# Kernel tuning notes

Hardware: AMD Instinct MI355X
Metric: run time of the kernel (lower is better)

## Reference

```python
import jax, jax.numpy as jnp
from jax import lax
import numpy as np

ALPHA = 1.5
N_ITER = 50  # default n_iter of entmax_bisect
NUM_HEADS = 16


def _entmax_bisect_p(X):
    """entmax-bisect over last axis (Peters et al. 2019 bisection algorithm)."""
    a = ALPHA
    inv = 1.0 / (a - 1.0)  # = 2.0 for alpha=1.5
    Xa = X * (a - 1.0)
    d = X.shape[-1]
    max_val = jnp.max(Xa, axis=-1, keepdims=True)
    tau_lo = max_val - 1.0
    tau_hi = max_val - (1.0 / d) ** (a - 1.0)
    f_lo = jnp.sum(jnp.clip(Xa - tau_lo, 0.0) ** inv, axis=-1, keepdims=True) - 1.0
    dm0 = tau_hi - tau_lo

    def body(carry, _):
        tau_lo, dm, _ = carry
        dm = dm * 0.5
        tau_m = tau_lo + dm
        p_m = jnp.clip(Xa - tau_m, 0.0) ** inv
        f_m = jnp.sum(p_m, axis=-1, keepdims=True) - 1.0
        tau_lo = jnp.where(f_m * f_lo >= 0, tau_m, tau_lo)
        return (tau_lo, dm, tau_m), None

    (tau_lo, dm, tau_m), _ = lax.scan(body, (tau_lo, dm0, tau_lo), None, length=N_ITER)
    p = jnp.clip(Xa - tau_m, 0.0) ** inv
    return p / jnp.sum(p, axis=-1, keepdims=True)  # ensure_sum_one


@jax.custom_vjp
def entmax_bisect(X):
    return _entmax_bisect_p(X)


def _entmax_fwd(X):
    p = _entmax_bisect_p(X)
    return p, p


def _entmax_bwd(p, dY):
    # exact entmax Jacobian-vector product (matches entmax package backward)
    gppr = jnp.where(p > 0, p ** (2.0 - ALPHA), 0.0)
    dX = dY * gppr
    q = jnp.sum(dX, axis=-1, keepdims=True) / jnp.sum(gppr, axis=-1, keepdims=True)
    return (dX - q * gppr,)


entmax_bisect.defvjp(_entmax_fwd, _entmax_bwd)


def setup_inputs() -> dict:
    key = jax.random.key(0)
    ks = jax.random.split(key, 9)
    B, N, C = 4, 1024, 1024
    s = 0.02
    return {
        "x": jax.random.normal(ks[0], (B, N, C), dtype=jnp.float32),
        "Wq": jax.random.normal(ks[1], (C, C), dtype=jnp.float32) * s,
        "bq": jnp.zeros((C,), dtype=jnp.float32),
        "Wk": jax.random.normal(ks[2], (C, C), dtype=jnp.float32) * s,
        "bk": jnp.zeros((C,), dtype=jnp.float32),
        "Wv": jax.random.normal(ks[3], (C, C), dtype=jnp.float32) * s,
        "bv": jnp.zeros((C,), dtype=jnp.float32),
        "Wo": jax.random.normal(ks[4], (C, C), dtype=jnp.float32) * s,
        "bo": jnp.zeros((C,), dtype=jnp.float32),
    }


def reference(x, Wq, bq, Wk, bk, Wv, bv, Wo, bo):
    B, N, C = x.shape
    H = NUM_HEADS
    Dh = C // H

    def split_heads(t):  # [B,N,C] -> [B,H,N,Dh]
        return t.reshape(B, N, H, Dh).transpose(0, 2, 1, 3)

    q = split_heads(x @ Wq + bq)
    k = split_heads(x @ Wk + bk)
    v = split_heads(x @ Wv + bv)

    scores = jnp.einsum("bhnd,bhmd->bhnm", q, k) / (float(Dh) ** 0.5)
    attn = entmax_bisect(scores)  # [B,H,N,N], sparse simplex weights
    out = jnp.einsum("bhnm,bhmd->bhnd", attn, v)
    out = out.transpose(0, 2, 1, 3).reshape(B, N, C)
    return out @ Wo + bo, attn
```

## Files before the change

### kernel.cpp

```cpp
#include <hip/hip_runtime.h>
#include <hip/hip_bf16.h>
#include <stdint.h>

#define NBAT 4
#define SEQ 1024
#define CH 1024
#define NH 16
#define DH 64
#define MTOT (NBAT*SEQ)

typedef __attribute__((ext_vector_type(8))) short bf16x8;
typedef __attribute__((ext_vector_type(4))) float f32x4;
typedef unsigned short u16;

#define FENCE() asm volatile("" ::: "memory")
#define BAR() do { FENCE(); __builtin_amdgcn_s_barrier(); FENCE(); } while (0)
#define WAIT_VM0() asm volatile("s_waitcnt vmcnt(0)" ::: "memory")
#define WAIT_VM2() asm volatile("s_waitcnt vmcnt(2)" ::: "memory")
#define WAIT_VM6() asm volatile("s_waitcnt vmcnt(6)" ::: "memory")
#define WAIT_LGKM0() asm volatile("s_waitcnt lgkmcnt(0)" ::: "memory")

__device__ __forceinline__ void g2l16(void* lds, const void* g) {
  __builtin_amdgcn_global_load_lds(
      (const __attribute__((address_space(1))) uint32_t*)g,
      (__attribute__((address_space(3))) uint32_t*)lds, 16, 0, 0);
}

__device__ __forceinline__ u16 f2bf(float f) {
  union { float f; uint32_t u; } v; v.f = f;
  uint32_t lsb = (v.u >> 16) & 1u;
  v.u += 0x7fffu + lsb;
  return (u16)(v.u >> 16);
}

__device__ __forceinline__ bf16x8 ldfrag(const u16* base, int row, int koff) {
  return *(const bf16x8*)((const char*)base + row * 128 + (koff ^ ((row & 7) << 4)));
}

__global__ __launch_bounds__(256) void cvt_x(const float* __restrict__ x,
                                             u16* __restrict__ xb) {
  int i = blockIdx.x * 256 + threadIdx.x;
  float4 v = ((const float4*)x)[i];
  ushort4 o;
  o.x = f2bf(v.x); o.y = f2bf(v.y); o.z = f2bf(v.z); o.w = f2bf(v.w);
  ((ushort4*)xb)[i] = o;
}

__global__ __launch_bounds__(256) void wt_bf16(const float* __restrict__ W,
                                               u16* __restrict__ Wt) {
  __shared__ u16 tile[64][65];
  const int bi = blockIdx.x;
  const int bj = blockIdx.y;
  const int t = threadIdx.x;
  const int c4 = (t & 15) * 4, rr = t >> 4;
#pragma unroll
  for (int p = 0; p < 4; p++) {
    int r = p * 16 + rr;
    float4 v = *(const float4*)(W + (size_t)(bj * 64 + r) * CH + bi * 64 + c4);
    tile[r][c4 + 0] = f2bf(v.x); tile[r][c4 + 1] = f2bf(v.y);
    tile[r][c4 + 2] = f2bf(v.z); tile[r][c4 + 3] = f2bf(v.w);
  }
  __syncthreads();
  const int n = t >> 2, ks = (t & 3) * 16;
  u16 tmp[16];
#pragma unroll
  for (int i = 0; i < 16; i++) tmp[i] = tile[ks + i][n];
#pragma unroll
  for (int s = 0; s < 4; s++) {
    ushort4 o; o.x = tmp[4*s]; o.y = tmp[4*s+1]; o.z = tmp[4*s+2]; o.w = tmp[4*s+3];
    *(ushort4*)(Wt + (size_t)(bi * 64 + n) * CH + bj * 64 + ks + 4 * s) = o;
  }
}

template<int MODE>
__global__ __launch_bounds__(256) void gemm128(
    const u16* __restrict__ A, const u16* __restrict__ Bt,
    const float* __restrict__ bias, void* __restrict__ outp)
{
  __shared__ u16 As[128 * 32];
  __shared__ u16 Bs[128 * 32];
  const int t = threadIdx.x;
  const int bn0 = blockIdx.x * 128;
  const int bm0 = blockIdx.y * 128;
  const int wid = t >> 6, lane = t & 63;
  const int wr = wid >> 1, wc = wid & 1;
  const int cl = lane & 15, g = lane >> 4;

  f32x4 acc[4][4] = {};
  const u16* ga = A  + (size_t)(bm0 + (t >> 2)) * CH + (t & 3) * 8;
  const u16* gb = Bt + (size_t)(bn0 + (t >> 2)) * CH + (t & 3) * 8;

  for (int k0 = 0; k0 < CH; k0 += 32) {
    g2l16(As + t * 8,        ga + k0);
    g2l16(As + 2048 + t * 8, ga + (size_t)64 * CH + k0);
    g2l16(Bs + t * 8,        gb + k0);
    g2l16(Bs + 2048 + t * 8, gb + (size_t)64 * CH + k0);
    __syncthreads();
    bf16x8 af[4], bfr[4];
#pragma unroll
    for (int f = 0; f < 4; f++) {
      af[f]  = *(const bf16x8*)(As + (wr * 64 + f * 16 + cl) * 32 + g * 8);
      bfr[f] = *(const bf16x8*)(Bs + (wc * 64 + f * 16 + cl) * 32 + g * 8);
    }
#pragma unroll
    for (int i = 0; i < 4; i++)
#pragma unroll
      for (int j = 0; j < 4; j++)
        acc[i][j] = __builtin_amdgcn_mfma_f32_16x16x32_bf16(af[i], bfr[j], acc[i][j], 0, 0, 0);
    __syncthreads();
  }

#pragma unroll
  for (int i = 0; i < 4; i++)
#pragma unroll
    for (int j = 0; j < 4; j++) {
      const int row0 = bm0 + wr * 64 + i * 16 + g * 4;
      const int col  = bn0 + wc * 64 + j * 16 + cl;
      const float bb = bias[col];
      f32x4 v = acc[i][j];
      if (MODE == 0) {
        u16* o = (u16*)outp;
#pragma unroll
        for (int q = 0; q < 4; q++) o[(size_t)(row0 + q) * CH + col] = f2bf(v[q] + bb);
      } else if (MODE == 1) {
        u16* o = (u16*)outp;
        ushort4 pk;
        pk.x = f2bf(v[0] + bb); pk.y = f2bf(v[1] + bb);
        pk.z = f2bf(v[2] + bb); pk.w = f2bf(v[3] + bb);
        *(ushort4*)(o + (size_t)col * MTOT + row0) = pk;
      } else {
        float* o = (float*)outp;
#pragma unroll
        for (int q = 0; q < 4; q++) o[(size_t)(row0 + q) * CH + col] = v[q] + bb;
      }
    }
}

__global__ __launch_bounds__(256, 3) void fused_attn(
    const u16* __restrict__ q, const u16* __restrict__ k,
    const u16* __restrict__ vt, float* __restrict__ attn,
    u16* __restrict__ o)
{
  __shared__ u16 buf[3][64 * 64];
  __shared__ u16 pcb[4 * 256];

  const int t = threadIdx.x;
  const int w = t >> 6, lane = t & 63;
  const int cl = lane & 15, g = lane >> 4;

  const int lin = blockIdx.x;
  const int u = lin >> 3;
  const int n0 = (u & 63) * 16;
  const int bh = (lin & 7) | ((u >> 6) << 3);
  const int b = bh >> 4, h = bh & 15;
  const int r0 = w * 4;

  const u16* qb = q  + ((size_t)(b * SEQ + n0) * CH + h * DH);
  const u16* kb = k  + ((size_t)(b * SEQ) * CH + h * DH);
  const u16* vb = vt + ((size_t)(h * DH) * MTOT + b * SEQ);

  const bf16x8 aq0 = *(const bf16x8*)(qb + (size_t)(r0 + (cl & 3)) * CH + g * 8);
  const bf16x8 aq1 = *(const bf16x8*)(qb + (size_t)(r0 + (cl & 3)) * CH + 32 + g * 8);

  const int srow = t >> 3;
  const int sbyte = ((t & 7) * 16) ^ ((srow & 7) << 4);
  const int scol = sbyte >> 1;

  g2l16(buf[0] + t * 8,        kb + (size_t)srow * CH + scol);
  g2l16(buf[0] + 2048 + t * 8, kb + (size_t)(srow + 32) * CH + scol);
  g2l16(buf[1] + t * 8,        kb + (size_t)(64 + srow) * CH + scol);
  g2l16(buf[1] + 2048 + t * 8, kb + (size_t)(64 + srow + 32) * CH + scol);

  float xa[4][16];

#pragma unroll
  for (int c = 0; c < 16; ++c) {
    WAIT_LGKM0();
    if (c < 15) { WAIT_VM2(); } else { WAIT_VM0(); }
    BAR();
    if (c + 2 < 16) {
      const u16* kc = kb + (size_t)(64 * (c + 2)) * CH;
      u16* d = buf[(c + 2) % 3];
      g2l16(d + t * 8,        kc + (size_t)srow * CH + scol);
      g2l16(d + 2048 + t * 8, kc + (size_t)(srow + 32) * CH + scol);
    }
    const u16* kc = buf[c % 3];
    f32x4 sc0 = {}, sc1 = {}, sc2 = {}, sc3 = {};
    sc0 = __builtin_amdgcn_mfma_f32_16x16x32_bf16(aq0, ldfrag(kc, cl,      g * 16), sc0, 0, 0, 0);
    sc0 = __builtin_amdgcn_mfma_f32_16x16x32_bf16(aq1, ldfrag(kc, cl,      64 + g * 16), sc0, 0, 0, 0);
    sc1 = __builtin_amdgcn_mfma_f32_16x16x32_bf16(aq0, ldfrag(kc, 16 + cl, g * 16), sc1, 0, 0, 0);
    sc1 = __builtin_amdgcn_mfma_f32_16x16x32_bf16(aq1, ldfrag(kc, 16 + cl, 64 + g * 16), sc1, 0, 0, 0);
    sc2 = __builtin_amdgcn_mfma_f32_16x16x32_bf16(aq0, ldfrag(kc, 32 + cl, g * 16), sc2, 0, 0, 0);
    sc2 = __builtin_amdgcn_mfma_f32_16x16x32_bf16(aq1, ldfrag(kc, 32 + cl, 64 + g * 16), sc2, 0, 0, 0);
    sc3 = __builtin_amdgcn_mfma_f32_16x16x32_bf16(aq0, ldfrag(kc, 48 + cl, g * 16), sc3, 0, 0, 0);
    sc3 = __builtin_amdgcn_mfma_f32_16x16x32_bf16(aq1, ldfrag(kc, 48 + cl, 64 + g * 16), sc3, 0, 0, 0);
#pragma unroll
    for (int qq = 0; qq < 4; ++qq) {
      float v = sc0[qq];
      v = (g == 1) ? sc1[qq] : v;
      v = (g == 2) ? sc2[qq] : v;
      v = (g == 3) ? sc3[qq] : v;
      xa[qq][c] = v * 0.0625f;
    }
  }

  g2l16(buf[1] + t * 8,        vb + (size_t)srow * MTOT + scol);
  g2l16(buf[1] + 2048 + t * 8, vb + (size_t)(srow + 32) * MTOT + scol);
  g2l16(buf[2] + t * 8,        vb + (size_t)srow * MTOT + 64 + scol);
  g2l16(buf[2] + 2048 + t * 8, vb + (size_t)(srow + 32) * MTOT + 64 + scol);

  float tau[4];
#pragma unroll
  for (int r = 0; r < 4; ++r) {
    float m = xa[r][0];
#pragma unroll
    for (int j = 1; j < 16; ++j) m = fmaxf(m, xa[r][j]);
#pragma unroll
    for (int off = 1; off < 64; off <<= 1) m = fmaxf(m, __shfl_xor(m, off));
    tau[r] = m - 1.0f;
  }
  for (int it = 0; it < 8; ++it) {
    float ss[4], sd[4];
#pragma unroll
    for (int r = 0; r < 4; ++r) {
      float s2 = 0.f, s1 = 0.f;
#pragma unroll
      for (int j = 0; j < 16; ++j) {
        float d = fmaxf(xa[r][j] - tau[r], 0.f);
        s2 = fmaf(d, d, s2); s1 += d;
      }
      ss[r] = s2; sd[r] = s1;
    }
#pragma unroll
    for (int off = 1; off < 64; off <<= 1) {
#pragma unroll
      for (int r = 0; r < 4; ++r) {
        ss[r] += __shfl_xor(ss[r], off);
        sd[r] += __shfl_xor(sd[r], off);
      }
    }
#pragma unroll
    for (int r = 0; r < 4; ++r)
      tau[r] += (ss[r] - 1.0f) / (sd[r] + sd[r]);
  }
  float inv[4];
#pragma unroll
  for (int r = 0; r < 4; ++r) {
    float s2 = 0.f;
#pragma unroll
    for (int j = 0; j < 16; ++j) { float d = fmaxf(xa[r][j] - tau[r], 0.f); s2 = fmaf(d, d, s2); }
#pragma unroll
    for (int off = 1; off < 64; off <<= 1) s2 += __shfl_xor(s2, off);
    inv[r] = 1.0f / s2;
  }

  char* pw = (char*)pcb + w * 512;
  f32x4 pva0 = {}, pva1 = {}, pva2 = {}, pva3 = {};
  float* ab = attn + (size_t)bh * SEQ * SEQ + (size_t)(n0 + r0) * SEQ;
#pragma unroll
  for (int vc = 0; vc < 16; ++vc) {
    float pval[4];
#pragma unroll
    for (int r = 0; r < 4; ++r) {
      float d = fmaxf(xa[r][vc] - tau[r], 0.f);
      pval[r] = d * d * inv[r];
      *(u16*)(pw + r * 128 + ((lane * 2) ^ (r << 4))) = f2bf(pval[r]);
    }
    WAIT_LGKM0();
    if (vc == 0) { WAIT_VM2(); } else { WAIT_VM6(); }
    BAR();
    if (vc + 2 < 16) {
      const u16* vc2 = vb + (size_t)64 * (vc + 2);
      u16* d = buf[(16 + vc + 2) % 3];
      g2l16(d + t * 8,        vc2 + (size_t)srow * MTOT + scol);
      g2l16(d + 2048 + t * 8, vc2 + (size_t)(srow + 32) * MTOT + scol);
    }
    const u16* vbu = buf[(16 + vc) % 3];
    const bf16x8 ap0 = *(const bf16x8*)(pw + (cl & 3) * 128 + ((g * 16) ^ ((cl & 3) << 4)));
    const bf16x8 ap1 = *(const bf16x8*)(pw + (cl & 3) * 128 + ((64 + g * 16) ^ ((cl & 3) << 4)));
    pva0 = __builtin_amdgcn_mfma_f32_16x16x32_bf16(ap0, ldfrag(vbu, cl,      g * 16), pva0, 0, 0, 0);
    pva0 = __builtin_amdgcn_mfma_f32_16x16x32_bf16(ap1, ldfrag(vbu, cl,      64 + g * 16), pva0, 0, 0, 0);
    pva1 = __builtin_amdgcn_mfma_f32_16x16x32_bf16(ap0, ldfrag(vbu, 16 + cl, g * 16), pva1, 0, 0, 0);
    pva1 = __builtin_amdgcn_mfma_f32_16x16x32_bf16(ap1, ldfrag(vbu, 16 + cl, 64 + g * 16), pva1, 0, 0, 0);
    pva2 = __builtin_amdgcn_mfma_f32_16x16x32_bf16(ap0, ldfrag(vbu, 32 + cl, g * 16), pva2, 0, 0, 0);
    pva2 = __builtin_amdgcn_mfma_f32_16x16x32_bf16(ap1, ldfrag(vbu, 32 + cl, 64 + g * 16), pva2, 0, 0, 0);
    pva3 = __builtin_amdgcn_mfma_f32_16x16x32_bf16(ap0, ldfrag(vbu, 48 + cl, g * 16), pva3, 0, 0, 0);
    pva3 = __builtin_amdgcn_mfma_f32_16x16x32_bf16(ap1, ldfrag(vbu, 48 + cl, 64 + g * 16), pva3, 0, 0, 0);
#pragma unroll
    for (int r = 0; r < 4; ++r)
      ab[(size_t)r * SEQ + vc * 64 + lane] = pval[r];
  }

  u16* ob = o + (size_t)(b * SEQ + n0 + r0) * CH + h * DH + lane;
#pragma unroll
  for (int qq = 0; qq < 4; ++qq) {
    float v = pva0[qq];
    v = (g == 1) ? pva1[qq] : v;
    v = (g == 2) ? pva2[qq] : v;
    v = (g == 3) ? pva3[qq] : v;
    ob[(size_t)qq * CH] = f2bf(v);
  }
}

extern "C" void kernel_launch(void* const* d_in, const int* in_sizes, int n_in,
                              void* d_out, int out_size, void* d_ws, size_t ws_size,
                              hipStream_t stream)
{
  const float* x  = (const float*)d_in[0];
  const float* Wq = (const float*)d_in[1];
  const float* bq = (const float*)d_in[2];
  const float* Wk = (const float*)d_in[3];
  const float* bk = (const float*)d_in[4];
  const float* Wv = (const float*)d_in[5];
  const float* bv = (const float*)d_in[6];
  const float* Wo = (const float*)d_in[7];
  const float* bo = (const float*)d_in[8];

  float* out0 = (float*)d_out;
  float* attn = out0 + (size_t)NBAT * SEQ * CH;

  const size_t T = (size_t)MTOT * CH;
  u16* xb  = (u16*)d_ws;
  u16* qw  = xb  + T;
  u16* kw  = qw  + T;
  u16* vtw = kw  + T;
  u16* ow  = vtw + T;
  u16* wtq = ow  + T;
  u16* wtk = wtq + (size_t)CH * CH;
  u16* wtv = wtk + (size_t)CH * CH;
  u16* wto = wtv + (size_t)CH * CH;

  cvt_x<<<T / (4 * 256), 256, 0, stream>>>(x, xb);
  wt_bf16<<<dim3(16, 16), 256, 0, stream>>>(Wq, wtq);
  wt_bf16<<<dim3(16, 16), 256, 0, stream>>>(Wk, wtk);
  wt_bf16<<<dim3(16, 16), 256, 0, stream>>>(Wv, wtv);
  wt_bf16<<<dim3(16, 16), 256, 0, stream>>>(Wo, wto);

  gemm128<0><<<dim3(CH / 128, MTOT / 128), 256, 0, stream>>>(xb, wtq, bq, qw);
  gemm128<0><<<dim3(CH / 128, MTOT / 128), 256, 0, stream>>>(xb, wtk, bk, kw);
  gemm128<1><<<dim3(CH / 128, MTOT / 128), 256, 0, stream>>>(xb, wtv, bv, vtw);

  fused_attn<<<4096, 256, 0, stream>>>(qw, kw, vtw, attn, ow);

  gemm128<2><<<dim3(CH / 128, MTOT / 128), 256, 0, stream>>>(ow, wto, bo, out0);
}
```

Baseline: 302.5 us.

## Merge QKV GEMMs into one launch, fold score scale into Q, trim iterations

The three QKV projection GEMMs are merged into a single launch using a z-dimension over the weights. The 1/sqrt(Dh) scale moves into the Q GEMM epilogue, so the attention kernel no longer multiplies every score. The attention kernel's launch-bound occupancy hint rises from 3 to 5 blocks, and the tau search loop drops from 8 to 7 iterations. Applying the scale before the bf16 rounding of Q changes rounding slightly. One fewer solver iteration may reduce the accuracy of the threshold.

```diff
diff --git a/kernel.cpp b/kernel.cpp
--- a/kernel.cpp
+++ b/kernel.cpp
@@ -73,15 +73,12 @@
 }
 
 template<int MODE>
-__global__ __launch_bounds__(256) void gemm128(
+__device__ __forceinline__ void gemm_body(
+    u16* As, u16* Bs,
     const u16* __restrict__ A, const u16* __restrict__ Bt,
-    const float* __restrict__ bias, void* __restrict__ outp)
-{
-  __shared__ u16 As[128 * 32];
-  __shared__ u16 Bs[128 * 32];
-  const int t = threadIdx.x;
-  const int bn0 = blockIdx.x * 128;
-  const int bm0 = blockIdx.y * 128;
+    const float* __restrict__ bias, void* __restrict__ outp,
+    float scale, int bn0, int bm0, int t)
+{
   const int wid = t >> 6, lane = t & 63;
   const int wr = wid >> 1, wc = wid & 1;
   const int cl = lane & 15, g = lane >> 4;
@@ -121,7 +118,7 @@
       if (MODE == 0) {
         u16* o = (u16*)outp;
 #pragma unroll
-        for (int q = 0; q < 4; q++) o[(size_t)(row0 + q) * CH + col] = f2bf(v[q] + bb);
+        for (int q = 0; q < 4; q++) o[(size_t)(row0 + q) * CH + col] = f2bf((v[q] + bb) * scale);
       } else if (MODE == 1) {
         u16* o = (u16*)outp;
         ushort4 pk;
@@ -136,7 +133,35 @@
     }
 }
 
-__global__ __launch_bounds__(256, 3) void fused_attn(
+__global__ __launch_bounds__(256) void gemm_qkv(
+    const u16* __restrict__ A,
+    const u16* __restrict__ Wtq, const float* __restrict__ bq, u16* __restrict__ qo,
+    const u16* __restrict__ Wtk, const float* __restrict__ bk, u16* __restrict__ ko,
+    const u16* __restrict__ Wtv, const float* __restrict__ bv, u16* __restrict__ vo)
+{
+  __shared__ u16 As[128 * 32];
+  __shared__ u16 Bs[128 * 32];
+  const int t = threadIdx.x;
+  const int bn0 = blockIdx.x * 128, bm0 = blockIdx.y * 128;
+  if (blockIdx.z == 0)
+    gemm_body<0>(As, Bs, A, Wtq, bq, qo, 0.0625f, bn0, bm0, t);
+  else if (blockIdx.z == 1)
+    gemm_body<0>(As, Bs, A, Wtk, bk, ko, 1.0f, bn0, bm0, t);
+  else
+    gemm_body<1>(As, Bs, A, Wtv, bv, vo, 1.0f, bn0, bm0, t);
+}
+
+__global__ __launch_bounds__(256) void gemm_out(
+    const u16* __restrict__ A, const u16* __restrict__ Bt,
+    const float* __restrict__ bias, float* __restrict__ outp)
+{
+  __shared__ u16 As[128 * 32];
+  __shared__ u16 Bs[128 * 32];
+  gemm_body<2>(As, Bs, A, Bt, bias, outp, 1.0f, blockIdx.x * 128, blockIdx.y * 128,
+               threadIdx.x);
+}
+
+__global__ __launch_bounds__(256, 5) void fused_attn(
     const u16* __restrict__ q, const u16* __restrict__ k,
     const u16* __restrict__ vt, float* __restrict__ attn,
     u16* __restrict__ o)
@@ -200,7 +225,7 @@
       v = (g == 1) ? sc1[qq] : v;
       v = (g == 2) ? sc2[qq] : v;
       v = (g == 3) ? sc3[qq] : v;
-      xa[qq][c] = v * 0.0625f;
+      xa[qq][c] = v;
     }
   }
 
@@ -219,7 +244,7 @@
     for (int off = 1; off < 64; off <<= 1) m = fmaxf(m, __shfl_xor(m, off));
     tau[r] = m - 1.0f;
   }
-  for (int it = 0; it < 8; ++it) {
+  for (int it = 0; it < 7; ++it) {
     float ss[4], sd[4];
 #pragma unroll
     for (int r = 0; r < 4; ++r) {
@@ -336,11 +361,10 @@
   wt_bf16<<<dim3(16, 16), 256, 0, stream>>>(Wv, wtv);
   wt_bf16<<<dim3(16, 16), 256, 0, stream>>>(Wo, wto);
 
-  gemm128<0><<<dim3(CH / 128, MTOT / 128), 256, 0, stream>>>(xb, wtq, bq, qw);
-  gemm128<0><<<dim3(CH / 128, MTOT / 128), 256, 0, stream>>>(xb, wtk, bk, kw);
-  gemm128<1><<<dim3(CH / 128, MTOT / 128), 256, 0, stream>>>(xb, wtv, bv, vtw);
+  gemm_qkv<<<dim3(CH / 128, MTOT / 128, 3), 256, 0, stream>>>(
+      xb, wtq, bq, qw, wtk, bk, kw, wtv, bv, vtw);
 
   fused_attn<<<4096, 256, 0, stream>>>(qw, kw, vtw, attn, ow);
 
-  gemm128<2><<<dim3(CH / 128, MTOT / 128), 256, 0, stream>>>(ow, wto, bo, out0);
-}
+  gemm_out<<<dim3(CH / 128, MTOT / 128), 256, 0, stream>>>(ow, wto, bo, out0);
+}
```

Result: faster. 288.7 us (-4.6%).
